# Optimization experiments

Measured on AMD Instinct MI355X. Metric: run time of the kernel, lower is better.

## Reference

```python
import jax, jax.numpy as jnp
import numpy as np

B, L, D, H, E, K = 2, 2048, 1024, 2048, 8, 2
NOISE_EPS = 0.01
CVLOSS, SWITCHLOSS, ZLOSS = 0.01, 0.1, 0.0001


def setup_inputs() -> dict:
    key = jax.random.key(0)
    k0, k1, k2, k3, k4 = jax.random.split(key, 5)
    x = jax.random.normal(k0, (B, L, D), jnp.float32)
    # gating weight (torch zero-inits; use small random so routing is nontrivial)
    w_gate = jax.random.normal(k1, (D, 2 * E), jnp.float32) * 0.02
    w1 = jax.random.normal(k2, (E, D, H), jnp.float32) * (1.0 / np.sqrt(D))
    w2 = jax.random.normal(k3, (E, H, D), jnp.float32) * (1.0 / np.sqrt(H))
    eps = jax.random.normal(k4, (B * L, E), jnp.float32)  # gating noise (randn_like)
    return {"x": x, "w_gate": w_gate, "w1": w1, "w2": w2, "eps": eps}


def moe_forward(x, w_gate, w1, w2, eps):
    b, l, d = x.shape
    T = b * l
    xf = x.reshape(T, d)                                   # [T, D]
    # --- noisy top-k gating ---
    clean, raw = jnp.split(xf @ w_gate, 2, axis=-1)        # each [T, E]
    noise_stddev = jax.nn.softplus(raw) + NOISE_EPS
    logits = clean + eps * noise_stddev
    probs = jax.nn.softmax(logits, axis=1)                 # [T, E]
    top_g, top_i = jax.lax.top_k(probs, K)                 # [T, K]
    rows = jnp.arange(T)[:, None]
    gates = jnp.zeros_like(probs).at[rows, top_i].set(top_g)  # dense gates [T, E]
    # --- aux losses (acc_aux_loss path disabled in source) ---
    expert_size = (gates > 0).sum(0).astype(jnp.float32)   # tokens per expert [E]
    g_sum = gates.sum(0)
    g_norm = g_sum / g_sum.sum()                           # F.normalize p=1
    cv = jnp.var(g_norm, ddof=1) / (jnp.mean(g_norm) ** 2 + 1e-10)  # torch unbiased var
    p_norm = probs.sum(0) / probs.sum()
    f_norm = expert_size / expert_size.sum()
    switch = (1.0 - (p_norm * f_norm).sum()) * E
    zl = jnp.mean(jax.nn.logsumexp(logits, axis=1) ** 2)
    loss = CVLOSS * cv + SWITCHLOSS * switch + ZLOSS * zl
    # --- expert compute + gated combine (grouped GEMM expressed as batched einsum;
    #     gates are zero off the top-k so math matches sort/dispatch/index_add) ---
    h = jax.nn.relu(jnp.einsum('td,edh->teh', xf, w1))     # [T, E, H]
    out = jnp.einsum('teh,ehd->ted', h, w2)                # [T, E, D]
    y = jnp.einsum('ted,te->td', out, gates)               # combine, multiply_by_gates
    return y.reshape(b, l, d), loss


def reference(x, w_gate, w1, w2, eps):
    return moe_forward(x, w_gate, w1, w2, eps)
```

## Files before the change

### kernel.cpp

```cpp
#include <hip/hip_runtime.h>

#define TT 4096
#define DD 1024
#define HH 2048
#define EE 8
#define TK 8192

typedef short  bf16x8 __attribute__((ext_vector_type(8)));
typedef float  f32x4  __attribute__((ext_vector_type(4)));

__device__ __forceinline__ unsigned short f2b(float f) {
    unsigned int u = __float_as_uint(f);
    unsigned int r = (u + 0x7fffu + ((u >> 16) & 1u)) >> 16;
    return (unsigned short)r;
}
__device__ __forceinline__ float b2f(unsigned short b) {
    return __uint_as_float(((unsigned int)b) << 16);
}

#define GLOAD_LDS16(SRC, DST) __builtin_amdgcn_global_load_lds( \
    (const __attribute__((address_space(1))) unsigned int*)(SRC), \
    (__attribute__((address_space(3))) unsigned int*)(DST), 16, 0, 0)

__global__ __launch_bounds__(256) void prep2(
    const float* __restrict__ w1, const float* __restrict__ w2,
    unsigned short* __restrict__ w1bT, unsigned short* __restrict__ w2bT,
    const float* __restrict__ x, const float* __restrict__ wg, const float* __restrict__ eps,
    float* __restrict__ stats_f, int* __restrict__ stats_i,
    int* __restrict__ top_i, float* __restrict__ top_g,
    unsigned short* __restrict__ xb) {
    __shared__ unsigned short tile[128][130];
    int b = blockIdx.x;
    if (b >= 1024) {
        int cb = b - 1024;
        const float* src; unsigned short* dst; int Kd, Nd, lb;
        if (cb < 1024) { src = w1; dst = w1bT; Kd = 1024; Nd = 2048; lb = cb; }
        else           { src = w2; dst = w2bT; Kd = 2048; Nd = 1024; lb = cb - 1024; }
        int nx = Nd >> 7, ny = Kd >> 7;
        int bx = lb % nx, by = (lb / nx) % ny, e = lb / (nx * ny);
        int n0 = bx * 128, k0 = by * 128;
        const float* s = src + (size_t)e * Kd * Nd;
        unsigned short* d = dst + (size_t)e * Kd * Nd;
        int rg = threadIdx.x >> 5;
        int c4 = (threadIdx.x & 31) * 4;
#pragma unroll
        for (int i = 0; i < 16; i++) {
            int r = rg + i * 8;
            float4 v = *(const float4*)(s + (size_t)(k0 + r) * Nd + n0 + c4);
            ushort2 lo, hi;
            lo.x = f2b(v.x); lo.y = f2b(v.y);
            hi.x = f2b(v.z); hi.y = f2b(v.w);
            *(ushort2*)(&tile[r][c4])     = lo;
            *(ushort2*)(&tile[r][c4 + 2]) = hi;
        }
        __syncthreads();
#pragma unroll
        for (int i = 0; i < 16; i++) {
            int n = rg + i * 8;
            ushort4 o;
            o.x = tile[c4 + 0][n];
            o.y = tile[c4 + 1][n];
            o.z = tile[c4 + 2][n];
            o.w = tile[c4 + 3][n];
            *(ushort4*)(d + (size_t)(n0 + n) * Kd + k0 + c4) = o;
        }
    } else {
        __shared__ float l_psum[8], l_gsum[8], l_zl;
        __shared__ int   l_cr[8], l_cp[8];
        int tid = threadIdx.x;
        if (tid < 8) { l_psum[tid] = 0.f; l_gsum[tid] = 0.f; l_cr[tid] = 0; l_cp[tid] = 0; }
        if (tid == 0) l_zl = 0.f;
        __syncthreads();
        int wave = tid >> 6, lane = tid & 63;
        int t = b * 4 + wave;
        const float* xr = x + (size_t)t * DD;
        unsigned short* xbr = xb + (size_t)t * DD;
#pragma unroll
        for (int i = 0; i < 4; i++) {
            int idx = lane + i * 64;
            float4 v = ((const float4*)xr)[idx];
            ushort4 o;
            o.x = f2b(v.x); o.y = f2b(v.y); o.z = f2b(v.z); o.w = f2b(v.w);
            ((ushort4*)xbr)[idx] = o;
        }
        int sub = lane >> 2, part = lane & 3;
        float a0 = 0.f, a1 = 0.f, a2 = 0.f, a3 = 0.f;
#pragma unroll 8
        for (int i = 0; i < 64; i++) {
            int dd = sub + i * 16;
            float xv = xr[dd];
            float4 w4 = *(const float4*)(wg + dd * 16 + part * 4);
            a0 += xv * w4.x; a1 += xv * w4.y; a2 += xv * w4.z; a3 += xv * w4.w;
        }
#pragma unroll
        for (int o = 4; o < 64; o <<= 1) {
            a0 += __shfl_xor(a0, o, 64);
            a1 += __shfl_xor(a1, o, 64);
            a2 += __shfl_xor(a2, o, 64);
            a3 += __shfl_xor(a3, o, 64);
        }
        float f16v[16];
#pragma unroll
        for (int src2 = 0; src2 < 4; src2++) {
            f16v[src2 * 4 + 0] = __shfl(a0, src2, 64);
            f16v[src2 * 4 + 1] = __shfl(a1, src2, 64);
            f16v[src2 * 4 + 2] = __shfl(a2, src2, 64);
            f16v[src2 * 4 + 3] = __shfl(a3, src2, 64);
        }
        if (lane == 0) {
            float lg[8], p[8];
            float mx = -1e30f;
            for (int e2 = 0; e2 < 8; e2++) {
                float raw = f16v[8 + e2];
                float sp = (raw > 20.f) ? raw : log1pf(__expf(raw));
                float l = f16v[e2] + eps[(size_t)t * 8 + e2] * (sp + 0.01f);
                lg[e2] = l; mx = fmaxf(mx, l);
            }
            float se = 0.f;
            for (int e2 = 0; e2 < 8; e2++) { p[e2] = __expf(lg[e2] - mx); se += p[e2]; }
            float lse = mx + logf(se);
            float inv = 1.f / se;
            for (int e2 = 0; e2 < 8; e2++) p[e2] *= inv;
            int i0 = 0;
            for (int e2 = 1; e2 < 8; e2++) if (p[e2] > p[i0]) i0 = e2;
            int i1 = (i0 == 0) ? 1 : 0;
            for (int e2 = 0; e2 < 8; e2++) if (e2 != i0 && p[e2] > p[i1]) i1 = e2;
            float g0 = p[i0], g1 = p[i1];
            top_i[t * 2] = i0; top_i[t * 2 + 1] = i1;
            top_g[t * 2] = g0; top_g[t * 2 + 1] = g1;
            for (int e2 = 0; e2 < 8; e2++) atomicAdd(&l_psum[e2], p[e2]);
            atomicAdd(&l_gsum[i0], g0); atomicAdd(&l_gsum[i1], g1);
            atomicAdd(&l_zl, lse * lse);
            atomicAdd(&l_cr[i0], 1); atomicAdd(&l_cr[i1], 1);
            if (g0 > 0.f) atomicAdd(&l_cp[i0], 1);
            if (g1 > 0.f) atomicAdd(&l_cp[i1], 1);
        }
        __syncthreads();
        if (tid < 8) {
            atomicAdd(&stats_f[tid],      l_psum[tid]);
            atomicAdd(&stats_f[8 + tid],  l_gsum[tid]);
            atomicAdd(&stats_i[tid],      l_cr[tid]);
            atomicAdd(&stats_i[8 + tid],  l_cp[tid]);
        }
        if (tid == 0) atomicAdd(&stats_f[16], l_zl);
    }
}

__global__ void scatter(const int* __restrict__ top_i, int* __restrict__ stats_i,
                        const float* __restrict__ stats_f,
                        int* __restrict__ row_token, int* __restrict__ pair_pos,
                        float* __restrict__ loss_out) {
    __shared__ int lcnt[8], lbase[8], soffs[9];
    int tid = threadIdx.x;
    if (tid < 8) lcnt[tid] = 0;
    if (tid == 0) {
        int off = 0;
        for (int e = 0; e < 8; e++) { soffs[e] = off; off += stats_i[e]; }
        soffs[8] = off;
    }
    __syncthreads();
    int t = blockIdx.x * 256 + tid;
    int e0 = top_i[t * 2], e1 = top_i[t * 2 + 1];
    int p0 = atomicAdd(&lcnt[e0], 1);
    int p1 = atomicAdd(&lcnt[e1], 1);
    __syncthreads();
    if (tid < 8) lbase[tid] = atomicAdd(&stats_i[16 + tid], lcnt[tid]);
    __syncthreads();
    int idx0 = soffs[e0] + lbase[e0] + p0;
    int idx1 = soffs[e1] + lbase[e1] + p1;
    row_token[idx0] = t;
    row_token[idx1] = t;
    pair_pos[t * 2] = idx0;
    pair_pos[t * 2 + 1] = idx1;
    if (blockIdx.x == 0 && tid == 0) {
        for (int e = 0; e < 9; e++) stats_i[24 + e] = soffs[e];
        float gs = 0.f;
        for (int e = 0; e < 8; e++) gs += stats_f[8 + e];
        float var = 0.f;
        for (int e = 0; e < 8; e++) {
            float gn = stats_f[8 + e] / gs;
            float d = gn - 0.125f;
            var += d * d;
        }
        var /= 7.f;
        float cv = var / (0.015625f + 1e-10f);
        float ps = 0.f, cs = 0.f;
        for (int e = 0; e < 8; e++) { ps += stats_f[e]; cs += (float)stats_i[8 + e]; }
        float dot = 0.f;
        for (int e = 0; e < 8; e++) dot += (stats_f[e] / ps) * ((float)stats_i[8 + e] / cs);
        float sw = (1.f - dot) * 8.f;
        float zl = stats_f[16] / (float)TT;
        *loss_out = 0.01f * cv + 0.1f * sw + 0.0001f * zl;
    }
}

template<int KTOT, int KSPLITS, int NTILES, bool GATHER, bool RELU>
__global__ __launch_bounds__(512, 1) void gemm_mt(
    const unsigned short* __restrict__ A,
    const unsigned short* __restrict__ Bt,
    unsigned short* __restrict__ C, long long split_stride,
    const int* __restrict__ row_token, const int* __restrict__ stats_i) {
    constexpr int KD   = KTOT / KSPLITS;
    constexpr int NK   = KD / 64;
    constexpr int NI   = NK / 2;
    constexpr int NDIM = NTILES * 256;
    static_assert(NTILES * KSPLITS == 8, "q must span 8");

    __shared__ __align__(16) unsigned short Al[2 * 256 * 64];
    __shared__ __align__(16) unsigned short Bl[2 * 256 * 64];

    const int* offs = stats_i + 24;
    int tid = threadIdx.x;
    int lane = tid & 63, wave = tid >> 6;

    if (blockIdx.x < 256) {
        int lin = blockIdx.x;
        int e   = lin & 7;
        int rem = lin >> 3;
        int q4  = rem & 7;
        int rt  = rem >> 3;
        int n0  = (q4 % NTILES) * 256;
        int split = q4 / NTILES;
        int off = offs[e];
        int ne  = offs[e + 1] - off;
        if (rt * 256 >= ne) return;

        int wm = wave >> 2, wn = wave & 3;

        const unsigned short* Asrc[4];
#pragma unroll
        for (int i = 0; i < 4; i++) {
            int glin = i * 512 + tid, row = glin >> 3, sl = glin & 7, g = sl ^ (row & 7);
            int arow;
            if (GATHER) arow = row_token[min(off + rt * 256 + row, TK - 1)];
            else        arow = min(off + rt * 256 + row, TK - 1);
            Asrc[i] = A + (size_t)arow * KTOT + split * KD + g * 8;
        }
        const unsigned short* Bte = Bt + (size_t)e * NDIM * KTOT;
        const unsigned short* Bsrc[4];
#pragma unroll
        for (int i = 0; i < 4; i++) {
            int glin = i * 512 + tid, row = glin >> 3, sl = glin & 7, g = sl ^ (row & 7);
            Bsrc[i] = Bte + (size_t)(n0 + row) * KTOT + split * KD + g * 8;
        }

        f32x4 acc[8][4];
#pragma unroll
        for (int m = 0; m < 8; m++)
#pragma unroll
            for (int n = 0; n < 4; n++)
#pragma unroll
                for (int i = 0; i < 4; i++) acc[m][n][i] = 0.f;

        bf16x8 bv[2][4], av[2][2];

#define STG_A(SLOT, KT, CC) GLOAD_LDS16(Asrc[CC] + (KT) * 64, Al + (SLOT) * 16384 + (CC) * 4096 + wave * 512)
#define STG_B(SLOT, KT, CC) GLOAD_LDS16(Bsrc[CC] + (KT) * 64, Bl + (SLOT) * 16384 + (CC) * 4096 + wave * 512)

#define LOAD_B(SLOT) do { \
    _Pragma("unroll") for (int kk2 = 0; kk2 < 2; kk2++) \
    _Pragma("unroll") for (int n = 0; n < 4; n++) { \
        int row = wn * 64 + n * 16 + (lane & 15); \
        int g = (kk2 * 4 + (lane >> 4)) ^ (row & 7); \
        bv[kk2][n] = *(const bf16x8*)(Bl + (SLOT) * 16384 + row * 64 + g * 8); \
    } } while (0)

#define LOAD_AQ(SLOT, QQ) do { \
    _Pragma("unroll") for (int kk2 = 0; kk2 < 2; kk2++) \
    _Pragma("unroll") for (int mi = 0; mi < 2; mi++) { \
        int row = wm * 128 + (QQ) * 32 + mi * 16 + (lane & 15); \
        int g = (kk2 * 4 + (lane >> 4)) ^ (row & 7); \
        av[kk2][mi] = *(const bf16x8*)(Al + (SLOT) * 16384 + row * 64 + g * 8); \
    } } while (0)

#define MFMA_Q(QQ) do { \
    _Pragma("unroll") for (int kk2 = 0; kk2 < 2; kk2++) \
    _Pragma("unroll") for (int mi = 0; mi < 2; mi++) \
    _Pragma("unroll") for (int n = 0; n < 4; n++) \
        acc[(QQ) * 2 + mi][n] = __builtin_amdgcn_mfma_f32_16x16x32_bf16(av[kk2][mi], bv[kk2][n], acc[(QQ) * 2 + mi][n], 0, 0, 0); \
    } while (0)

#define PHASE(SLOT, QQ, STAGE_STMT, WAIT_STMT) do { \
    if ((QQ) == 0) LOAD_B(SLOT); \
    LOAD_AQ(SLOT, QQ); \
    STAGE_STMT; \
    __builtin_amdgcn_s_barrier(); \
    asm volatile("s_waitcnt lgkmcnt(0)" ::: "memory"); \
    __builtin_amdgcn_s_setprio(1); \
    MFMA_Q(QQ); \
    __builtin_amdgcn_s_setprio(0); \
    WAIT_STMT; \
    __builtin_amdgcn_s_barrier(); \
    } while (0)

#pragma unroll
        for (int c = 0; c < 4; c++) STG_B(0, 0, c);
#pragma unroll
        for (int c = 0; c < 4; c++) STG_A(0, 0, c);
#pragma unroll
        for (int c = 0; c < 4; c++) STG_B(1, 1, c);
        STG_A(1, 1, 0); STG_A(1, 1, 2);
        asm volatile("s_waitcnt vmcnt(6)" ::: "memory");
        __builtin_amdgcn_s_barrier();

#pragma unroll 1
        for (int it = 0; it < NI; ++it) {
            int u = 2 * it, v = u + 1;
            bool ns = (it + 1 < NI);
            PHASE(0, 0, { STG_A(1, v, 1); STG_A(1, v, 3); }, {});
            PHASE(0, 1, { if (ns) { STG_B(0, u + 2, 0); STG_B(0, u + 2, 1); } }, {});
            PHASE(0, 2, { if (ns) { STG_B(0, u + 2, 2); STG_B(0, u + 2, 3); } }, {});
            PHASE(0, 3, { if (ns) { STG_A(0, u + 2, 0); STG_A(0, u + 2, 2); } },
                        { if (ns) asm volatile("s_waitcnt vmcnt(6)" ::: "memory");
                          else    asm volatile("s_waitcnt vmcnt(0)" ::: "memory"); });
            PHASE(1, 0, { if (ns) { STG_A(0, u + 2, 1); STG_A(0, u + 2, 3); } }, {});
            PHASE(1, 1, { if (ns) { STG_B(1, v + 2, 0); STG_B(1, v + 2, 1); } }, {});
            PHASE(1, 2, { if (ns) { STG_B(1, v + 2, 2); STG_B(1, v + 2, 3); } }, {});
            PHASE(1, 3, { if (ns) { STG_A(1, v + 2, 0); STG_A(1, v + 2, 2); } },
                        { if (ns) asm volatile("s_waitcnt vmcnt(6)" ::: "memory"); });
        }
#undef PHASE
#undef MFMA_Q
#undef LOAD_AQ
#undef LOAD_B
#undef STG_A
#undef STG_B

        unsigned short* Cb = C + (ptrdiff_t)split * split_stride;
#pragma unroll
        for (int m = 0; m < 8; m++) {
            int rr0 = rt * 256 + wm * 128 + m * 16 + (lane >> 4) * 4;
#pragma unroll
            for (int i = 0; i < 4; i++) {
                if (rr0 + i < ne) {
                    size_t grow = (size_t)(off + rr0 + i);
#pragma unroll
                    for (int n = 0; n < 4; n++) {
                        int col = n0 + wn * 64 + n * 16 + (lane & 15);
                        float vvv = acc[m][n][i];
                        if (RELU) vvv = fmaxf(vvv, 0.f);
                        Cb[grow * NDIM + col] = f2b(vvv);
                    }
                }
            }
        }
    } else {
        int t   = blockIdx.x - 256;
        int e   = t & 7;
        int rem = t >> 3;
        int q4  = rem & 7;
        int s0  = rem >> 3;
        int n0  = (q4 % NTILES) * 256;
        int split = q4 / NTILES;
        int off = offs[e];
        int ne  = offs[e + 1] - off;
        int m0  = 1024 + s0 * 64;
        if (m0 >= ne) return;

        int wm = wave >> 2, wn = wave & 3;

        const unsigned short* Asrc;
        {
            int row = tid >> 3, sl = tid & 7, g = sl ^ (row & 7);
            int arow;
            if (GATHER) arow = row_token[min(off + m0 + row, TK - 1)];
            else        arow = min(off + m0 + row, TK - 1);
            Asrc = A + (size_t)arow * KTOT + split * KD + g * 8;
        }
        const unsigned short* Bte = Bt + (size_t)e * NDIM * KTOT;
        const unsigned short* Bsrc[4];
#pragma unroll
        for (int i = 0; i < 4; i++) {
            int glin = i * 512 + tid, row = glin >> 3, sl = glin & 7, g = sl ^ (row & 7);
            Bsrc[i] = Bte + (size_t)(n0 + row) * KTOT + split * KD + g * 8;
        }

        f32x4 acc2[2][4];
#pragma unroll
        for (int m = 0; m < 2; m++)
#pragma unroll
            for (int n = 0; n < 4; n++)
#pragma unroll
                for (int i = 0; i < 4; i++) acc2[m][n][i] = 0.f;

#define TTSG(S, KT) do { \
    unsigned short* Ab_ = Al + (S) * 4096; \
    unsigned short* Bb_ = ((S) == 2) ? (Al + 16384) : (Bl + (S) * 16384); \
    GLOAD_LDS16(Asrc + (KT) * 64, Ab_ + wave * 512); \
    _Pragma("unroll") for (int c_ = 0; c_ < 4; c_++) \
        GLOAD_LDS16(Bsrc[c_] + (KT) * 64, Bb_ + c_ * 4096 + wave * 512); \
} while (0)

        TTSG(0, 0);
        TTSG(1, 1);
        int sb = 0;
#pragma unroll 1
        for (int kt = 0; kt < NK; ++kt) {
            if (kt + 1 < NK) asm volatile("s_waitcnt vmcnt(5)" ::: "memory");
            else             asm volatile("s_waitcnt vmcnt(0)" ::: "memory");
            __builtin_amdgcn_s_barrier();
            if (kt + 2 < NK) { int s2 = sb + 2; if (s2 >= 3) s2 -= 3; TTSG(s2, kt + 2); }
            const unsigned short* Ab = Al + sb * 4096;
            const unsigned short* Bb = (sb == 2) ? (Al + 16384) : (Bl + sb * 16384);
            bf16x8 a2[2][2], b2[2][4];
#pragma unroll
            for (int kk2 = 0; kk2 < 2; kk2++) {
#pragma unroll
                for (int mi = 0; mi < 2; mi++) {
                    int row = wm * 32 + mi * 16 + (lane & 15);
                    int g = (kk2 * 4 + (lane >> 4)) ^ (row & 7);
                    a2[kk2][mi] = *(const bf16x8*)(Ab + row * 64 + g * 8);
                }
#pragma unroll
                for (int n = 0; n < 4; n++) {
                    int row = wn * 64 + n * 16 + (lane & 15);
                    int g = (kk2 * 4 + (lane >> 4)) ^ (row & 7);
                    b2[kk2][n] = *(const bf16x8*)(Bb + row * 64 + g * 8);
                }
            }
#pragma unroll
            for (int kk2 = 0; kk2 < 2; kk2++)
#pragma unroll
                for (int mi = 0; mi < 2; mi++)
#pragma unroll
                    for (int n = 0; n < 4; n++)
                        acc2[mi][n] = __builtin_amdgcn_mfma_f32_16x16x32_bf16(a2[kk2][mi], b2[kk2][n], acc2[mi][n], 0, 0, 0);
            sb = (sb == 2) ? 0 : sb + 1;
        }
#undef TTSG

        unsigned short* Cb = C + (ptrdiff_t)split * split_stride;
#pragma unroll
        for (int mi = 0; mi < 2; mi++) {
            int rr0 = m0 + wm * 32 + mi * 16 + (lane >> 4) * 4;
#pragma unroll
            for (int i = 0; i < 4; i++) {
                if (rr0 + i < ne) {
                    size_t grow = (size_t)(off + rr0 + i);
#pragma unroll
                    for (int n = 0; n < 4; n++) {
                        int col = n0 + wn * 64 + n * 16 + (lane & 15);
                        float vvv = acc2[mi][n][i];
                        if (RELU) vvv = fmaxf(vvv, 0.f);
                        Cb[grow * NDIM + col] = f2b(vvv);
                    }
                }
            }
        }
    }
}

__global__ void combine(const unsigned short* __restrict__ o0,
                        const unsigned short* __restrict__ o1,
                        const int* __restrict__ pair_pos, const float* __restrict__ top_g,
                        float* __restrict__ y) {
    int t = blockIdx.x;
    int tid = threadIdx.x;
    int i0 = pair_pos[t * 2], i1 = pair_pos[t * 2 + 1];
    float g0 = top_g[t * 2], g1 = top_g[t * 2 + 1];
    int d0 = tid * 4;
    ushort4 a0 = *(const ushort4*)(o0 + (size_t)i0 * DD + d0);
    ushort4 a1 = *(const ushort4*)(o1 + (size_t)i0 * DD + d0);
    ushort4 b0 = *(const ushort4*)(o0 + (size_t)i1 * DD + d0);
    ushort4 b1 = *(const ushort4*)(o1 + (size_t)i1 * DD + d0);
    float4 o;
    o.x = g0 * (b2f(a0.x) + b2f(a1.x)) + g1 * (b2f(b0.x) + b2f(b1.x));
    o.y = g0 * (b2f(a0.y) + b2f(a1.y)) + g1 * (b2f(b0.y) + b2f(b1.y));
    o.z = g0 * (b2f(a0.z) + b2f(a1.z)) + g1 * (b2f(b0.z) + b2f(b1.z));
    o.w = g0 * (b2f(a0.w) + b2f(a1.w)) + g1 * (b2f(b0.w) + b2f(b1.w));
    *(float4*)(y + (size_t)t * DD + d0) = o;
}

extern "C" void kernel_launch(void* const* d_in, const int* in_sizes, int n_in,
                              void* d_out, int out_size, void* d_ws, size_t ws_size,
                              hipStream_t stream) {
    const float* x   = (const float*)d_in[0];
    const float* wg  = (const float*)d_in[1];
    const float* w1  = (const float*)d_in[2];
    const float* w2  = (const float*)d_in[3];
    const float* eps = (const float*)d_in[4];
    float* y = (float*)d_out;
    char* ws = (char*)d_ws;

    unsigned short* xb    = (unsigned short*)(ws);
    unsigned short* w1bT  = (unsigned short*)(ws + 8388608);
    unsigned short* w2bT  = (unsigned short*)(ws + 41943040);
    unsigned short* hbuf  = (unsigned short*)(ws + 75497472);
    unsigned short* outp0 = (unsigned short*)(ws + 109051904);
    unsigned short* outp1 = (unsigned short*)(ws + 8388608);
    int*   top_i    = (int*)(ws + 125829120);
    float* top_g    = (float*)(ws + 125861888);
    int*   row_token= (int*)(ws + 125894656);
    int*   pair_pos = (int*)(ws + 125927424);
    float* stats_f  = (float*)(ws + 125960192);
    int*   stats_i  = (int*)(ws + 125960192 + 128);

    hipMemsetAsync(ws + 125960192, 0, 768, stream);
    prep2<<<3072, 256, 0, stream>>>(w1, w2, w1bT, w2bT, x, wg, eps,
                                    stats_f, stats_i, top_i, top_g, xb);
    scatter<<<16, 256, 0, stream>>>(top_i, stats_i, stats_f, row_token, pair_pos, y + (size_t)TT * DD);
    gemm_mt<1024, 1, 8, true,  true ><<<512, 512, 0, stream>>>(
        xb, w1bT, hbuf, 0, row_token, stats_i);
    gemm_mt<2048, 2, 4, false, false><<<512, 512, 0, stream>>>(
        hbuf, w2bT, outp0, (long long)(outp1 - outp0), row_token, stats_i);
    combine<<<4096, 256, 0, stream>>>(outp0, outp1, pair_pos, top_g, y);
}
```

Measured before the change: 182.2 us.

## Replace split-K second expert GEMM with dedicated full-K 128x256 tiled kernel

The second grouped GEMM previously split K in two and wrote two partial bf16 outputs that the combine kernel summed. A new kernel computes the full K=2048 reduction per tile, using a 128x256 tile with a multi-phase double-buffered LDS pipeline for the first 1024 rows of each expert and a 64-row tail path for the rest. Combine now reads a single output buffer, which halves its gather traffic and removes the partial-sum round trip. In exchange each block runs a longer K loop with fewer blocks, which may reduce parallelism for unevenly sized experts.

```diff
diff --git a/kernel.cpp b/kernel.cpp
--- a/kernel.cpp
+++ b/kernel.cpp
@@ -450,8 +450,245 @@
     }
 }
 
-__global__ void combine(const unsigned short* __restrict__ o0,
-                        const unsigned short* __restrict__ o1,
+__global__ __launch_bounds__(512, 1) void gemm2f(
+    const unsigned short* __restrict__ A,
+    const unsigned short* __restrict__ Bt,
+    unsigned short* __restrict__ C,
+    const int* __restrict__ row_token, const int* __restrict__ stats_i) {
+    constexpr int KTOT = 2048, NDIM = 1024;
+    constexpr int NK = 32, NI = 16;
+
+    __shared__ __align__(16) unsigned short Al[2 * 128 * 64];
+    __shared__ __align__(16) unsigned short Bl[2 * 256 * 64];
+
+    const int* offs = stats_i + 24;
+    int tid = threadIdx.x;
+    int lane = tid & 63, wave = tid >> 6;
+    int wm = wave >> 2, wn = wave & 3;
+
+    if (blockIdx.x < 256) {
+        int lin = blockIdx.x;
+        int e   = lin & 7;
+        int rem = lin >> 3;
+        int q4  = rem & 3;
+        int rt  = rem >> 2;
+        int n0  = q4 * 256;
+        int off = offs[e];
+        int ne  = offs[e + 1] - off;
+        if (rt * 128 >= ne) return;
+
+        const unsigned short* Asrc[2];
+#pragma unroll
+        for (int i = 0; i < 2; i++) {
+            int glin = i * 512 + tid, row = glin >> 3, sl = glin & 7, g = sl ^ (row & 7);
+            int arow = min(off + rt * 128 + row, TK - 1);
+            Asrc[i] = A + (size_t)arow * KTOT + g * 8;
+        }
+        const unsigned short* Bte = Bt + (size_t)e * NDIM * KTOT;
+        const unsigned short* Bsrc[4];
+#pragma unroll
+        for (int i = 0; i < 4; i++) {
+            int glin = i * 512 + tid, row = glin >> 3, sl = glin & 7, g = sl ^ (row & 7);
+            Bsrc[i] = Bte + (size_t)(n0 + row) * KTOT + g * 8;
+        }
+
+        f32x4 acc[4][4];
+#pragma unroll
+        for (int m = 0; m < 4; m++)
+#pragma unroll
+            for (int n = 0; n < 4; n++)
+#pragma unroll
+                for (int i = 0; i < 4; i++) acc[m][n][i] = 0.f;
+
+        bf16x8 bv[2][4], av[2];
+
+#define S2A(SLOT, KT, CC) GLOAD_LDS16(Asrc[CC] + (KT) * 64, Al + (SLOT) * 8192 + (CC) * 4096 + wave * 512)
+#define S2B(SLOT, KT, CC) GLOAD_LDS16(Bsrc[CC] + (KT) * 64, Bl + (SLOT) * 16384 + (CC) * 4096 + wave * 512)
+
+#define LD2B(SLOT) do { \
+    _Pragma("unroll") for (int kk2 = 0; kk2 < 2; kk2++) \
+    _Pragma("unroll") for (int n = 0; n < 4; n++) { \
+        int row = wn * 64 + n * 16 + (lane & 15); \
+        int g = (kk2 * 4 + (lane >> 4)) ^ (row & 7); \
+        bv[kk2][n] = *(const bf16x8*)(Bl + (SLOT) * 16384 + row * 64 + g * 8); \
+    } } while (0)
+
+#define LD2A(SLOT, QQ) do { \
+    _Pragma("unroll") for (int kk2 = 0; kk2 < 2; kk2++) { \
+        int row = wm * 64 + (QQ) * 16 + (lane & 15); \
+        int g = (kk2 * 4 + (lane >> 4)) ^ (row & 7); \
+        av[kk2] = *(const bf16x8*)(Al + (SLOT) * 8192 + row * 64 + g * 8); \
+    } } while (0)
+
+#define MM2(QQ) do { \
+    _Pragma("unroll") for (int kk2 = 0; kk2 < 2; kk2++) \
+    _Pragma("unroll") for (int n = 0; n < 4; n++) \
+        acc[QQ][n] = __builtin_amdgcn_mfma_f32_16x16x32_bf16(av[kk2], bv[kk2][n], acc[QQ][n], 0, 0, 0); \
+    } while (0)
+
+#define PH2(SLOT, QQ, STAGE_STMT, WAIT_STMT) do { \
+    if ((QQ) == 0) LD2B(SLOT); \
+    LD2A(SLOT, QQ); \
+    STAGE_STMT; \
+    __builtin_amdgcn_s_barrier(); \
+    asm volatile("s_waitcnt lgkmcnt(0)" ::: "memory"); \
+    __builtin_amdgcn_s_setprio(1); \
+    MM2(QQ); \
+    __builtin_amdgcn_s_setprio(0); \
+    WAIT_STMT; \
+    __builtin_amdgcn_s_barrier(); \
+    } while (0)
+
+#pragma unroll
+        for (int c = 0; c < 4; c++) S2B(0, 0, c);
+        S2A(0, 0, 0); S2A(0, 0, 1);
+#pragma unroll
+        for (int c = 0; c < 4; c++) S2B(1, 1, c);
+        asm volatile("s_waitcnt vmcnt(4)" ::: "memory");
+        __builtin_amdgcn_s_barrier();
+
+#pragma unroll 1
+        for (int it = 0; it < NI; ++it) {
+            int u = 2 * it, v = u + 1;
+            bool ns = (it + 1 < NI);
+            PH2(0, 0, { S2A(1, v, 0); }, {});
+            PH2(0, 1, { S2A(1, v, 1); if (ns) { S2B(0, u + 2, 0); S2B(0, u + 2, 1); } }, {});
+            PH2(0, 2, { if (ns) { S2B(0, u + 2, 2); S2B(0, u + 2, 3); } }, {});
+            PH2(0, 3, {}, { if (ns) asm volatile("s_waitcnt vmcnt(4)" ::: "memory");
+                            else    asm volatile("s_waitcnt vmcnt(0)" ::: "memory"); });
+            PH2(1, 0, { if (ns) { S2A(0, u + 2, 0); S2A(0, u + 2, 1); } }, {});
+            PH2(1, 1, { if (ns) { S2B(1, v + 2, 0); S2B(1, v + 2, 1); } }, {});
+            PH2(1, 2, { if (ns) { S2B(1, v + 2, 2); S2B(1, v + 2, 3); } }, {});
+            PH2(1, 3, {}, { if (ns) asm volatile("s_waitcnt vmcnt(4)" ::: "memory");
+                            else    asm volatile("s_waitcnt vmcnt(0)" ::: "memory"); });
+        }
+#undef PH2
+#undef MM2
+#undef LD2A
+#undef LD2B
+#undef S2A
+#undef S2B
+
+#pragma unroll
+        for (int m = 0; m < 4; m++) {
+            int rr0 = rt * 128 + wm * 64 + m * 16 + (lane >> 4) * 4;
+#pragma unroll
+            for (int i = 0; i < 4; i++) {
+                if (rr0 + i < ne) {
+                    size_t grow = (size_t)(off + rr0 + i);
+#pragma unroll
+                    for (int n = 0; n < 4; n++) {
+                        int col = n0 + wn * 64 + n * 16 + (lane & 15);
+                        C[grow * NDIM + col] = f2b(acc[m][n][i]);
+                    }
+                }
+            }
+        }
+    } else {
+        int t   = blockIdx.x - 256;
+        int e   = t & 7;
+        int rem = t >> 3;
+        int q4  = rem & 7;
+        int s0  = rem >> 3;
+        if (q4 >= 4) return;
+        int n0  = q4 * 256;
+        int off = offs[e];
+        int ne  = offs[e + 1] - off;
+        int m0  = 1024 + s0 * 64;
+        if (m0 >= ne) return;
+
+        const unsigned short* Asrc;
+        {
+            int row = tid >> 3, sl = tid & 7, g = sl ^ (row & 7);
+            int arow = min(off + m0 + row, TK - 1);
+            Asrc = A + (size_t)arow * KTOT + g * 8;
+        }
+        const unsigned short* Bte = Bt + (size_t)e * NDIM * KTOT;
+        const unsigned short* Bsrc[4];
+#pragma unroll
+        for (int i = 0; i < 4; i++) {
+            int glin = i * 512 + tid, row = glin >> 3, sl = glin & 7, g = sl ^ (row & 7);
+            Bsrc[i] = Bte + (size_t)(n0 + row) * KTOT + g * 8;
+        }
+
+        f32x4 acc2[2][4];
+#pragma unroll
+        for (int m = 0; m < 2; m++)
+#pragma unroll
+            for (int n = 0; n < 4; n++)
+#pragma unroll
+                for (int i = 0; i < 4; i++) acc2[m][n][i] = 0.f;
+
+#define TTSG2(S, KT) do { \
+    unsigned short* Ab_ = Al + (S) * 4096; \
+    unsigned short* Bb_ = ((S) == 2) ? (Al + 12288) : (Bl + (S) * 16384); \
+    GLOAD_LDS16(Asrc + (KT) * 64, Ab_ + wave * 512); \
+    _Pragma("unroll") for (int c_ = 0; c_ < 4; c_++) \
+        GLOAD_LDS16(Bsrc[c_] + (KT) * 64, Bb_ + c_ * 4096 + wave * 512); \
+} while (0)
+#undef TTSG2
+
+#define TSTG(BUF, KT) do { \
+    GLOAD_LDS16(Asrc + (KT) * 64, Al + (BUF) * 4096 + wave * 512); \
+    _Pragma("unroll") for (int c_ = 0; c_ < 4; c_++) \
+        GLOAD_LDS16(Bsrc[c_] + (KT) * 64, Bl + (BUF) * 16384 + c_ * 4096 + wave * 512); \
+} while (0)
+
+        TSTG(0, 0);
+        asm volatile("s_waitcnt vmcnt(0)" ::: "memory");
+        __builtin_amdgcn_s_barrier();
+
+#pragma unroll 1
+        for (int kt = 0; kt < NK; ++kt) {
+            if (kt + 1 < NK) TSTG((kt & 1) ^ 1, kt + 1);
+            int B = kt & 1;
+            bf16x8 a2[2][2], b2[2][4];
+#pragma unroll
+            for (int kk2 = 0; kk2 < 2; kk2++) {
+#pragma unroll
+                for (int mi = 0; mi < 2; mi++) {
+                    int row = wm * 32 + mi * 16 + (lane & 15);
+                    int g = (kk2 * 4 + (lane >> 4)) ^ (row & 7);
+                    a2[kk2][mi] = *(const bf16x8*)(Al + B * 4096 + row * 64 + g * 8);
+                }
+#pragma unroll
+                for (int n = 0; n < 4; n++) {
+                    int row = wn * 64 + n * 16 + (lane & 15);
+                    int g = (kk2 * 4 + (lane >> 4)) ^ (row & 7);
+                    b2[kk2][n] = *(const bf16x8*)(Bl + B * 16384 + row * 64 + g * 8);
+                }
+            }
+#pragma unroll
+            for (int kk2 = 0; kk2 < 2; kk2++)
+#pragma unroll
+                for (int mi = 0; mi < 2; mi++)
+#pragma unroll
+                    for (int n = 0; n < 4; n++)
+                        acc2[mi][n] = __builtin_amdgcn_mfma_f32_16x16x32_bf16(a2[kk2][mi], b2[kk2][n], acc2[mi][n], 0, 0, 0);
+            asm volatile("s_waitcnt vmcnt(0) lgkmcnt(0)" ::: "memory");
+            __builtin_amdgcn_s_barrier();
+        }
+#undef TSTG
+
+#pragma unroll
+        for (int mi = 0; mi < 2; mi++) {
+            int rr0 = m0 + wm * 32 + mi * 16 + (lane >> 4) * 4;
+#pragma unroll
+            for (int i = 0; i < 4; i++) {
+                if (rr0 + i < ne) {
+                    size_t grow = (size_t)(off + rr0 + i);
+#pragma unroll
+                    for (int n = 0; n < 4; n++) {
+                        int col = n0 + wn * 64 + n * 16 + (lane & 15);
+                        C[grow * NDIM + col] = f2b(acc2[mi][n][i]);
+                    }
+                }
+            }
+        }
+    }
+}
+
+__global__ void combine(const unsigned short* __restrict__ outp,
                         const int* __restrict__ pair_pos, const float* __restrict__ top_g,
                         float* __restrict__ y) {
     int t = blockIdx.x;
@@ -459,15 +696,13 @@
     int i0 = pair_pos[t * 2], i1 = pair_pos[t * 2 + 1];
     float g0 = top_g[t * 2], g1 = top_g[t * 2 + 1];
     int d0 = tid * 4;
-    ushort4 a0 = *(const ushort4*)(o0 + (size_t)i0 * DD + d0);
-    ushort4 a1 = *(const ushort4*)(o1 + (size_t)i0 * DD + d0);
-    ushort4 b0 = *(const ushort4*)(o0 + (size_t)i1 * DD + d0);
-    ushort4 b1 = *(const ushort4*)(o1 + (size_t)i1 * DD + d0);
+    ushort4 a = *(const ushort4*)(outp + (size_t)i0 * DD + d0);
+    ushort4 b = *(const ushort4*)(outp + (size_t)i1 * DD + d0);
     float4 o;
-    o.x = g0 * (b2f(a0.x) + b2f(a1.x)) + g1 * (b2f(b0.x) + b2f(b1.x));
-    o.y = g0 * (b2f(a0.y) + b2f(a1.y)) + g1 * (b2f(b0.y) + b2f(b1.y));
-    o.z = g0 * (b2f(a0.z) + b2f(a1.z)) + g1 * (b2f(b0.z) + b2f(b1.z));
-    o.w = g0 * (b2f(a0.w) + b2f(a1.w)) + g1 * (b2f(b0.w) + b2f(b1.w));
+    o.x = g0 * b2f(a.x) + g1 * b2f(b.x);
+    o.y = g0 * b2f(a.y) + g1 * b2f(b.y);
+    o.z = g0 * b2f(a.z) + g1 * b2f(b.z);
+    o.w = g0 * b2f(a.w) + g1 * b2f(b.w);
     *(float4*)(y + (size_t)t * DD + d0) = o;
 }
 
@@ -486,8 +721,7 @@
     unsigned short* w1bT  = (unsigned short*)(ws + 8388608);
     unsigned short* w2bT  = (unsigned short*)(ws + 41943040);
     unsigned short* hbuf  = (unsigned short*)(ws + 75497472);
-    unsigned short* outp0 = (unsigned short*)(ws + 109051904);
-    unsigned short* outp1 = (unsigned short*)(ws + 8388608);
+    unsigned short* outp  = (unsigned short*)(ws + 109051904);
     int*   top_i    = (int*)(ws + 125829120);
     float* top_g    = (float*)(ws + 125861888);
     int*   row_token= (int*)(ws + 125894656);
@@ -501,7 +735,6 @@
     scatter<<<16, 256, 0, stream>>>(top_i, stats_i, stats_f, row_token, pair_pos, y + (size_t)TT * DD);
     gemm_mt<1024, 1, 8, true,  true ><<<512, 512, 0, stream>>>(
         xb, w1bT, hbuf, 0, row_token, stats_i);
-    gemm_mt<2048, 2, 4, false, false><<<512, 512, 0, stream>>>(
-        hbuf, w2bT, outp0, (long long)(outp1 - outp0), row_token, stats_i);
-    combine<<<4096, 256, 0, stream>>>(outp0, outp1, pair_pos, top_g, y);
+    gemm2f<<<512, 512, 0, stream>>>(hbuf, w2bT, outp, row_token, stats_i);
+    combine<<<4096, 256, 0, stream>>>(outp, pair_pos, top_g, y);
 }
```

Measured after the change: 198.4 us. 8.9% more time.
